# Kernel optimization log

Measured on AMD Instinct MI355X. Metric: run time of the kernel, lower is better.

The kernel has to match this reference:

```python
import jax, jax.numpy as jnp
import numpy as np

N = 40000      # nodes
E = 640000     # edges (avg degree 16)
IN = 128
H = 128
OUT = 64


def setup_inputs() -> dict:
    key = jax.random.key(0)
    ks = jax.random.split(key, 10)
    s_in = 1.0 / np.sqrt(IN)
    s_h = 1.0 / np.sqrt(H)
    return {
        "x": jax.random.normal(ks[0], (N, IN), jnp.float32),
        "edge_index": jax.random.randint(ks[1], (2, E), 0, N, dtype=jnp.int64),
        "W1l": jax.random.normal(ks[2], (IN, H), jnp.float32) * s_in,
        "W1r": jax.random.normal(ks[3], (IN, H), jnp.float32) * s_in,
        "b1": jnp.zeros((H,), jnp.float32),
        "W2l": jax.random.normal(ks[4], (H, H), jnp.float32) * s_h,
        "W2r": jax.random.normal(ks[5], (H, H), jnp.float32) * s_h,
        "b2": jnp.zeros((H,), jnp.float32),
        "Wout": jax.random.normal(ks[6], (H, OUT), jnp.float32) * s_h,
        "bout": jnp.zeros((OUT,), jnp.float32),
    }


def _sage_conv(x, src, dst, Wl, Wr, b):
    # mean aggregation of source features onto destination nodes
    msg = x[src]                                   # [E, d] gather
    agg = jax.ops.segment_sum(msg, dst, num_segments=N)       # [N, d]
    deg = jax.ops.segment_sum(jnp.ones((src.shape[0],), x.dtype), dst,
                              num_segments=N)                  # [N]
    agg = agg / jnp.maximum(deg, 1.0)[:, None]
    # PyG SAGEConv: lin_l(aggregated neighbors) + lin_r(root); bias on lin_l
    return agg @ Wl + x @ Wr + b


def reference(x, edge_index, W1l, W1r, b1, W2l, W2r, b2, Wout, bout):
    src, dst = edge_index[0], edge_index[1]
    h = jax.nn.relu(_sage_conv(x, src, dst, W1l, W1r, b1))
    h = jax.nn.relu(_sage_conv(h, src, dst, W2l, W2r, b2))
    return h @ Wout + bout
```

## Files before the change

### kernel.cpp

```cpp
#include <hip/hip_runtime.h>


typedef __attribute__((ext_vector_type(8))) short short8v;
typedef __attribute__((ext_vector_type(4))) float f32x4;
typedef __attribute__((ext_vector_type(4))) _Float16 half4v;
typedef __attribute__((ext_vector_type(8))) _Float16 half8v;

#define CAP 64

static __device__ __forceinline__ unsigned short f2bf(float f) {
  unsigned u = __float_as_uint(f);
  u += 0x7fffu + ((u >> 16) & 1u);
  return (unsigned short)(u >> 16);
}
static __device__ __forceinline__ float bf2f(unsigned short h) {
  return __uint_as_float(((unsigned)h) << 16);
}

__global__ __launch_bounds__(256) void k_setup(
    const int* __restrict__ src, const int* __restrict__ dst,
    int* __restrict__ cnt, ushort* __restrict__ csr,
    const float* __restrict__ W1l, const float* __restrict__ W1r,
    const float* __restrict__ W2l, const float* __restrict__ W2r,
    ushort* __restrict__ w1h, ushort* __restrict__ w1lo,
    ushort* __restrict__ w2h, ushort* __restrict__ w2lo,
    const float* __restrict__ Wout, ushort* __restrict__ woh,
    ushort* __restrict__ wol, const float* __restrict__ x,
    _Float16* __restrict__ xh, int E, int N) {
  int t = blockIdx.x * 256 + threadIdx.x;
  if (t < E) {
    int d = dst[t];
    int pos = atomicAdd(&cnt[d], 1);
    if (pos < CAP) csr[(size_t)d * CAP + pos] = (ushort)src[t];
    return;
  }
  t -= E;
  if (t < 8192) {
    const bool is2 = t >= 4096;
    int u = t & 4095;
    const float* Wl = is2 ? W2l : W1l;
    const float* Wr = is2 ? W2r : W1r;
    ushort* wh = is2 ? w2h : w1h;
    ushort* wlo = is2 ? w2lo : w1lo;
    int l = u & 63;
    int n = (u >> 6) & 7;
    int s = u >> 9;
    int col = n * 16 + (l & 15);
    int kb = s * 32 + ((l >> 4) * 8);
    size_t base = ((size_t)(s * 8 + n) * 64 + l) * 8;
#pragma unroll
    for (int j = 0; j < 8; ++j) {
      int k = kb + j;
      float w = (k < 128) ? Wl[(size_t)k * 128 + col] : Wr[(size_t)(k - 128) * 128 + col];
      unsigned short hb = f2bf(w);
      wh[base + j] = hb;
      wlo[base + j] = f2bf(w - bf2f(hb));
    }
    return;
  }
  t -= 8192;
  if (t < 1024) {
    int l = t & 63;
    int n = (t >> 6) & 3;
    int s = t >> 8;
    int col = n * 16 + (l & 15);
    int kb = s * 32 + ((l >> 4) * 8);
    size_t base = ((size_t)(s * 4 + n) * 64 + l) * 8;
#pragma unroll
    for (int j = 0; j < 8; ++j) {
      float w = Wout[(size_t)(kb + j) * 64 + col];
      unsigned short hb = f2bf(w);
      woh[base + j] = hb;
      wol[base + j] = f2bf(w - bf2f(hb));
    }
    return;
  }
  t -= 1024;
  if (t < N * 32) {
    float4 v = reinterpret_cast<const float4*>(x)[t];
    half4v o = {(_Float16)v.x, (_Float16)v.y, (_Float16)v.z, (_Float16)v.w};
    reinterpret_cast<half4v*>(xh)[t] = o;
  }
}

__global__ __launch_bounds__(256) void k_agg(const _Float16* __restrict__ feat,
                                             const int* __restrict__ cnt,
                                             const ushort* __restrict__ csr,
                                             _Float16* __restrict__ agg, int N) {
  int node = (blockIdx.x * 256 + threadIdx.x) >> 6;
  if (node >= N) return;
  const int lane = threadIdx.x & 63;
  const int q = lane >> 4;
  const int c = (lane & 15) * 8;
  const int deg = cnt[node];
  const int stored = deg < CAP ? deg : CAP;
  const ushort* idx = csr + (size_t)node * CAP;
  float a0[8] = {}, a1[8] = {}, a2[8] = {}, a3[8] = {};
  for (int j = 0; j < stored; j += 16) {
    int r0 = j + q, r1 = j + 4 + q, r2 = j + 8 + q, r3 = j + 12 + q;
    if (r0 < stored) {
      int i0 = idx[r0];
      half8v v = *reinterpret_cast<const half8v*>(feat + (size_t)i0 * 128 + c);
#pragma unroll
      for (int t = 0; t < 8; ++t) a0[t] += (float)v[t];
    }
    if (r1 < stored) {
      int i1 = idx[r1];
      half8v v = *reinterpret_cast<const half8v*>(feat + (size_t)i1 * 128 + c);
#pragma unroll
      for (int t = 0; t < 8; ++t) a1[t] += (float)v[t];
    }
    if (r2 < stored) {
      int i2 = idx[r2];
      half8v v = *reinterpret_cast<const half8v*>(feat + (size_t)i2 * 128 + c);
#pragma unroll
      for (int t = 0; t < 8; ++t) a2[t] += (float)v[t];
    }
    if (r3 < stored) {
      int i3 = idx[r3];
      half8v v = *reinterpret_cast<const half8v*>(feat + (size_t)i3 * 128 + c);
#pragma unroll
      for (int t = 0; t < 8; ++t) a3[t] += (float)v[t];
    }
  }
  float s[8];
#pragma unroll
  for (int t = 0; t < 8; ++t) {
    s[t] = (a0[t] + a1[t]) + (a2[t] + a3[t]);
    s[t] += __shfl_xor(s[t], 16);
    s[t] += __shfl_xor(s[t], 32);
  }
  if (lane < 16) {
    float invd = 1.0f / fmaxf((float)deg, 1.0f);
    half8v o;
#pragma unroll
    for (int t = 0; t < 8; ++t) o[t] = (_Float16)(s[t] * invd);
    *reinterpret_cast<half8v*>(agg + (size_t)node * 128 + c) = o;
  }
}

__global__ __launch_bounds__(256) void k_gemm1(
    const _Float16* __restrict__ aggh, const float* __restrict__ rootf,
    const ushort* __restrict__ wh, const ushort* __restrict__ wl_,
    const float* __restrict__ bias, _Float16* __restrict__ outh, int M) {
  const int lane = threadIdx.x & 63;
  const int wave = threadIdx.x >> 6;
  const int row = blockIdx.x * 64 + wave * 16;
  f32x4 acc[8] = {};

  for (int s = 0; s < 8; ++s) {
    const int kb = (s & 3) * 32;
    const size_t aoff = (size_t)(row + (lane & 15)) * 128 + kb + (lane >> 4) * 8;
    float av[8];
    if (s < 4) {
      half8v hv = *reinterpret_cast<const half8v*>(aggh + aoff);
#pragma unroll
      for (int j = 0; j < 8; ++j) av[j] = (float)hv[j];
    } else {
      float4 av0 = *reinterpret_cast<const float4*>(rootf + aoff);
      float4 av1 = *reinterpret_cast<const float4*>(rootf + aoff + 4);
      av[0] = av0.x; av[1] = av0.y; av[2] = av0.z; av[3] = av0.w;
      av[4] = av1.x; av[5] = av1.y; av[6] = av1.z; av[7] = av1.w;
    }
    short8v ah, al;
#pragma unroll
    for (int j = 0; j < 8; ++j) {
      unsigned short hb = f2bf(av[j]);
      ah[j] = (short)hb;
      al[j] = (short)f2bf(av[j] - bf2f(hb));
    }
    const size_t sbase = (size_t)s * 8 * 64 * 8 + (size_t)lane * 8;
#pragma unroll
    for (int n = 0; n < 8; ++n) {
      short8v bh = *reinterpret_cast<const short8v*>(wh + sbase + (size_t)n * 64 * 8);
      short8v bl = *reinterpret_cast<const short8v*>(wl_ + sbase + (size_t)n * 64 * 8);
      acc[n] = __builtin_amdgcn_mfma_f32_16x16x32_bf16(ah, bh, acc[n], 0, 0, 0);
      acc[n] = __builtin_amdgcn_mfma_f32_16x16x32_bf16(ah, bl, acc[n], 0, 0, 0);
      acc[n] = __builtin_amdgcn_mfma_f32_16x16x32_bf16(al, bh, acc[n], 0, 0, 0);
    }
  }

  const int r0 = row + (lane >> 4) * 4;
  const int col0 = lane & 15;
#pragma unroll
  for (int n = 0; n < 8; ++n) {
    int col = n * 16 + col0;
    float bv = bias[col];
#pragma unroll
    for (int r = 0; r < 4; ++r) {
      float v = fmaxf(acc[n][r] + bv, 0.f);
      outh[(size_t)(r0 + r) * 128 + col] = (_Float16)v;
    }
  }
}

__global__ __launch_bounds__(256) void k_gemm2_out(
    const _Float16* __restrict__ aggh, const _Float16* __restrict__ rooth,
    const ushort* __restrict__ w2h, const ushort* __restrict__ w2l,
    const float* __restrict__ b2, const ushort* __restrict__ woh,
    const ushort* __restrict__ wol, const float* __restrict__ bout,
    float* __restrict__ out, int M) {
  __shared__ float H[64][132];
  const int lane = threadIdx.x & 63;
  const int wave = threadIdx.x >> 6;
  const int row = blockIdx.x * 64 + wave * 16;
  f32x4 acc[8] = {};

  for (int s = 0; s < 8; ++s) {
    const int kb = (s & 3) * 32;
    const size_t aoff = (size_t)(row + (lane & 15)) * 128 + kb + (lane >> 4) * 8;
    const _Float16* ap = (s < 4) ? (aggh + aoff) : (rooth + aoff);
    half8v hv = *reinterpret_cast<const half8v*>(ap);
    float av[8];
#pragma unroll
    for (int j = 0; j < 8; ++j) av[j] = (float)hv[j];
    short8v ah, al;
#pragma unroll
    for (int j = 0; j < 8; ++j) {
      unsigned short hb = f2bf(av[j]);
      ah[j] = (short)hb;
      al[j] = (short)f2bf(av[j] - bf2f(hb));
    }
    const size_t sbase = (size_t)s * 8 * 64 * 8 + (size_t)lane * 8;
#pragma unroll
    for (int n = 0; n < 8; ++n) {
      short8v bh = *reinterpret_cast<const short8v*>(w2h + sbase + (size_t)n * 64 * 8);
      short8v bl = *reinterpret_cast<const short8v*>(w2l + sbase + (size_t)n * 64 * 8);
      acc[n] = __builtin_amdgcn_mfma_f32_16x16x32_bf16(ah, bh, acc[n], 0, 0, 0);
      acc[n] = __builtin_amdgcn_mfma_f32_16x16x32_bf16(ah, bl, acc[n], 0, 0, 0);
      acc[n] = __builtin_amdgcn_mfma_f32_16x16x32_bf16(al, bh, acc[n], 0, 0, 0);
    }
  }

  const int r0loc = wave * 16 + (lane >> 4) * 4;
  const int col0 = lane & 15;
#pragma unroll
  for (int n = 0; n < 8; ++n) {
    int col = n * 16 + col0;
    float bv = b2[col];
#pragma unroll
    for (int r = 0; r < 4; ++r) {
      H[r0loc + r][col] = fmaxf(acc[n][r] + bv, 0.f);
    }
  }
  __syncthreads();

  f32x4 acc2[4] = {};
  for (int s = 0; s < 4; ++s) {
    const float* hp = &H[wave * 16 + (lane & 15)][s * 32 + (lane >> 4) * 8];
    float av[8];
#pragma unroll
    for (int j = 0; j < 8; ++j) av[j] = hp[j];
    short8v ah, al;
#pragma unroll
    for (int j = 0; j < 8; ++j) {
      unsigned short hb = f2bf(av[j]);
      ah[j] = (short)hb;
      al[j] = (short)f2bf(av[j] - bf2f(hb));
    }
    const size_t sbase = (size_t)s * 4 * 64 * 8 + (size_t)lane * 8;
#pragma unroll
    for (int n = 0; n < 4; ++n) {
      short8v bh = *reinterpret_cast<const short8v*>(woh + sbase + (size_t)n * 64 * 8);
      short8v bl = *reinterpret_cast<const short8v*>(wol + sbase + (size_t)n * 64 * 8);
      acc2[n] = __builtin_amdgcn_mfma_f32_16x16x32_bf16(ah, bh, acc2[n], 0, 0, 0);
      acc2[n] = __builtin_amdgcn_mfma_f32_16x16x32_bf16(ah, bl, acc2[n], 0, 0, 0);
      acc2[n] = __builtin_amdgcn_mfma_f32_16x16x32_bf16(al, bh, acc2[n], 0, 0, 0);
    }
  }

  const int r0 = row + (lane >> 4) * 4;
#pragma unroll
  for (int n = 0; n < 4; ++n) {
    int col = n * 16 + col0;
    float bv = bout[col];
#pragma unroll
    for (int r = 0; r < 4; ++r) {
      out[(size_t)(r0 + r) * 64 + col] = acc2[n][r] + bv;
    }
  }
}

extern "C" void kernel_launch(void* const* d_in, const int* in_sizes, int n_in,
                              void* d_out, int out_size, void* d_ws, size_t ws_size,
                              hipStream_t stream) {
  const float* x    = (const float*)d_in[0];
  const int*   ei   = (const int*)d_in[1];
  const float* W1l  = (const float*)d_in[2];
  const float* W1r  = (const float*)d_in[3];
  const float* b1   = (const float*)d_in[4];
  const float* W2l  = (const float*)d_in[5];
  const float* W2r  = (const float*)d_in[6];
  const float* b2   = (const float*)d_in[7];
  const float* Wout = (const float*)d_in[8];
  const float* bout = (const float*)d_in[9];
  float* out = (float*)d_out;

  const int N = in_sizes[0] / 128;
  const int E = in_sizes[1] / 2;
  const int* src = ei;
  const int* dst = ei + E;

  auto align = [](size_t b) { return (b + 255) & ~(size_t)255; };
  char* p = (char*)d_ws;
  int* cnt       = (int*)p;       p += align((size_t)N * 4);
  ushort* csr    = (ushort*)p;    p += align((size_t)N * CAP * 2);
  _Float16* xh   = (_Float16*)p;  p += align((size_t)N * 128 * 2);
  _Float16* aggh = (_Float16*)p;  p += align((size_t)N * 128 * 2);
  ushort* w1h    = (ushort*)p;    p += align(32768 * 2);
  ushort* w1lo   = (ushort*)p;    p += align(32768 * 2);
  ushort* w2h    = (ushort*)p;    p += align(32768 * 2);
  ushort* w2lo   = (ushort*)p;    p += align(32768 * 2);
  ushort* woh    = (ushort*)p;    p += align(8192 * 2);
  ushort* wol    = (ushort*)p;    p += align(8192 * 2);
  _Float16* h1h  = xh;

  (void)hipMemsetAsync(cnt, 0, (size_t)N * 4, stream);

  const int gemmBlocks = (N + 63) / 64;
  const int aggBlocks = (N + 3) / 4;
  const int setupThreads = E + 8192 + 1024 + N * 32;

  k_setup<<<(setupThreads + 255) / 256, 256, 0, stream>>>(
      src, dst, cnt, csr, W1l, W1r, W2l, W2r, w1h, w1lo, w2h, w2lo,
      Wout, woh, wol, x, xh, E, N);

  k_agg<<<aggBlocks, 256, 0, stream>>>(xh, cnt, csr, aggh, N);
  k_gemm1<<<gemmBlocks, 256, 0, stream>>>(aggh, x, w1h, w1lo, b1, h1h, N);

  k_agg<<<aggBlocks, 256, 0, stream>>>(h1h, cnt, csr, aggh, N);
  k_gemm2_out<<<gemmBlocks, 256, 0, stream>>>(aggh, h1h, w2h, w2lo, b2,
                                              woh, wol, bout, out, N);
}
```

Measured before the change: 152.8 us.

## Map 16 lanes per node in aggregation and read fp16 root features in gemm1

The aggregation kernel now gives each node 16 lanes instead of a full wave, so one wave handles 4 nodes. Each lane issues up to 8 independent neighbor gathers per iteration, and the cross-lane shuffle reduction is removed. gemm1 now reads the root term from the fp16 copy of x instead of fp32, which halves that read traffic but loses precision on the root input. h1 gets its own buffer rather than aliasing xh, which adds workspace memory. Lane groups in a wave can now have different degrees, so some lanes may sit idle when degrees are uneven.

```diff
diff --git a/kernel.cpp b/kernel.cpp
--- a/kernel.cpp
+++ b/kernel.cpp
@@ -87,60 +87,52 @@
                                              const int* __restrict__ cnt,
                                              const ushort* __restrict__ csr,
                                              _Float16* __restrict__ agg, int N) {
-  int node = (blockIdx.x * 256 + threadIdx.x) >> 6;
-  if (node >= N) return;
   const int lane = threadIdx.x & 63;
   const int q = lane >> 4;
   const int c = (lane & 15) * 8;
+  const int wave = threadIdx.x >> 6;
+  const int node0 = blockIdx.x * 16 + wave * 4 + q;
+  const bool valid = node0 < N;
+  const int node = valid ? node0 : (N - 1);
   const int deg = cnt[node];
   const int stored = deg < CAP ? deg : CAP;
   const ushort* idx = csr + (size_t)node * CAP;
-  float a0[8] = {}, a1[8] = {}, a2[8] = {}, a3[8] = {};
-  for (int j = 0; j < stored; j += 16) {
-    int r0 = j + q, r1 = j + 4 + q, r2 = j + 8 + q, r3 = j + 12 + q;
-    if (r0 < stored) {
-      int i0 = idx[r0];
-      half8v v = *reinterpret_cast<const half8v*>(feat + (size_t)i0 * 128 + c);
-#pragma unroll
-      for (int t = 0; t < 8; ++t) a0[t] += (float)v[t];
-    }
-    if (r1 < stored) {
-      int i1 = idx[r1];
-      half8v v = *reinterpret_cast<const half8v*>(feat + (size_t)i1 * 128 + c);
-#pragma unroll
-      for (int t = 0; t < 8; ++t) a1[t] += (float)v[t];
-    }
-    if (r2 < stored) {
-      int i2 = idx[r2];
-      half8v v = *reinterpret_cast<const half8v*>(feat + (size_t)i2 * 128 + c);
-#pragma unroll
-      for (int t = 0; t < 8; ++t) a2[t] += (float)v[t];
-    }
-    if (r3 < stored) {
-      int i3 = idx[r3];
-      half8v v = *reinterpret_cast<const half8v*>(feat + (size_t)i3 * 128 + c);
-#pragma unroll
-      for (int t = 0; t < 8; ++t) a3[t] += (float)v[t];
-    }
-  }
-  float s[8];
-#pragma unroll
-  for (int t = 0; t < 8; ++t) {
-    s[t] = (a0[t] + a1[t]) + (a2[t] + a3[t]);
-    s[t] += __shfl_xor(s[t], 16);
-    s[t] += __shfl_xor(s[t], 32);
-  }
-  if (lane < 16) {
+  float a[8] = {};
+  for (int j = 0; j < stored; j += 8) {
+    half8v v0, v1, v2, v3, v4, v5, v6, v7;
+    if (j + 0 < stored) { int nb = idx[j + 0]; v0 = *reinterpret_cast<const half8v*>(feat + (size_t)nb * 128 + c); }
+    if (j + 1 < stored) { int nb = idx[j + 1]; v1 = *reinterpret_cast<const half8v*>(feat + (size_t)nb * 128 + c); }
+    if (j + 2 < stored) { int nb = idx[j + 2]; v2 = *reinterpret_cast<const half8v*>(feat + (size_t)nb * 128 + c); }
+    if (j + 3 < stored) { int nb = idx[j + 3]; v3 = *reinterpret_cast<const half8v*>(feat + (size_t)nb * 128 + c); }
+    if (j + 4 < stored) { int nb = idx[j + 4]; v4 = *reinterpret_cast<const half8v*>(feat + (size_t)nb * 128 + c); }
+    if (j + 5 < stored) { int nb = idx[j + 5]; v5 = *reinterpret_cast<const half8v*>(feat + (size_t)nb * 128 + c); }
+    if (j + 6 < stored) { int nb = idx[j + 6]; v6 = *reinterpret_cast<const half8v*>(feat + (size_t)nb * 128 + c); }
+    if (j + 7 < stored) { int nb = idx[j + 7]; v7 = *reinterpret_cast<const half8v*>(feat + (size_t)nb * 128 + c); }
+#pragma unroll
+    for (int t = 0; t < 8; ++t) {
+      float s0 = 0.f, s1 = 0.f;
+      if (j + 0 < stored) s0 += (float)v0[t];
+      if (j + 1 < stored) s1 += (float)v1[t];
+      if (j + 2 < stored) s0 += (float)v2[t];
+      if (j + 3 < stored) s1 += (float)v3[t];
+      if (j + 4 < stored) s0 += (float)v4[t];
+      if (j + 5 < stored) s1 += (float)v5[t];
+      if (j + 6 < stored) s0 += (float)v6[t];
+      if (j + 7 < stored) s1 += (float)v7[t];
+      a[t] += s0 + s1;
+    }
+  }
+  if (valid) {
     float invd = 1.0f / fmaxf((float)deg, 1.0f);
     half8v o;
 #pragma unroll
-    for (int t = 0; t < 8; ++t) o[t] = (_Float16)(s[t] * invd);
+    for (int t = 0; t < 8; ++t) o[t] = (_Float16)(a[t] * invd);
     *reinterpret_cast<half8v*>(agg + (size_t)node * 128 + c) = o;
   }
 }
 
 __global__ __launch_bounds__(256) void k_gemm1(
-    const _Float16* __restrict__ aggh, const float* __restrict__ rootf,
+    const _Float16* __restrict__ aggh, const _Float16* __restrict__ rooth,
     const ushort* __restrict__ wh, const ushort* __restrict__ wl_,
     const float* __restrict__ bias, _Float16* __restrict__ outh, int M) {
   const int lane = threadIdx.x & 63;
@@ -151,17 +143,11 @@
   for (int s = 0; s < 8; ++s) {
     const int kb = (s & 3) * 32;
     const size_t aoff = (size_t)(row + (lane & 15)) * 128 + kb + (lane >> 4) * 8;
+    const _Float16* ap = (s < 4) ? (aggh + aoff) : (rooth + aoff);
+    half8v hv = *reinterpret_cast<const half8v*>(ap);
     float av[8];
-    if (s < 4) {
-      half8v hv = *reinterpret_cast<const half8v*>(aggh + aoff);
-#pragma unroll
-      for (int j = 0; j < 8; ++j) av[j] = (float)hv[j];
-    } else {
-      float4 av0 = *reinterpret_cast<const float4*>(rootf + aoff);
-      float4 av1 = *reinterpret_cast<const float4*>(rootf + aoff + 4);
-      av[0] = av0.x; av[1] = av0.y; av[2] = av0.z; av[3] = av0.w;
-      av[4] = av1.x; av[5] = av1.y; av[6] = av1.z; av[7] = av1.w;
-    }
+#pragma unroll
+    for (int j = 0; j < 8; ++j) av[j] = (float)hv[j];
     short8v ah, al;
 #pragma unroll
     for (int j = 0; j < 8; ++j) {
@@ -306,6 +292,7 @@
   int* cnt       = (int*)p;       p += align((size_t)N * 4);
   ushort* csr    = (ushort*)p;    p += align((size_t)N * CAP * 2);
   _Float16* xh   = (_Float16*)p;  p += align((size_t)N * 128 * 2);
+  _Float16* h1h  = (_Float16*)p;  p += align((size_t)N * 128 * 2);
   _Float16* aggh = (_Float16*)p;  p += align((size_t)N * 128 * 2);
   ushort* w1h    = (ushort*)p;    p += align(32768 * 2);
   ushort* w1lo   = (ushort*)p;    p += align(32768 * 2);
@@ -313,12 +300,11 @@
   ushort* w2lo   = (ushort*)p;    p += align(32768 * 2);
   ushort* woh    = (ushort*)p;    p += align(8192 * 2);
   ushort* wol    = (ushort*)p;    p += align(8192 * 2);
-  _Float16* h1h  = xh;
 
   (void)hipMemsetAsync(cnt, 0, (size_t)N * 4, stream);
 
   const int gemmBlocks = (N + 63) / 64;
-  const int aggBlocks = (N + 3) / 4;
+  const int aggBlocks = (N + 15) / 16;
   const int setupThreads = E + 8192 + 1024 + N * 32;
 
   k_setup<<<(setupThreads + 255) / 256, 256, 0, stream>>>(
@@ -326,7 +312,7 @@
       Wout, woh, wol, x, xh, E, N);
 
   k_agg<<<aggBlocks, 256, 0, stream>>>(xh, cnt, csr, aggh, N);
-  k_gemm1<<<gemmBlocks, 256, 0, stream>>>(aggh, x, w1h, w1lo, b1, h1h, N);
+  k_gemm1<<<gemmBlocks, 256, 0, stream>>>(aggh, xh, w1h, w1lo, b1, h1h, N);
 
   k_agg<<<aggBlocks, 256, 0, stream>>>(h1h, cnt, csr, aggh, N);
   k_gemm2_out<<<gemmBlocks, 256, 0, stream>>>(aggh, h1h, w2h, w2lo, b2,
```

New measurement: 148.4 us. 1.03x faster.
